# Kernel tuning notes

Hardware: AMD Instinct MI355X
Metric: run time of the kernel (lower is better)

## Reference

```python
import jax, jax.numpy as jnp
import numpy as np

GAMMA = 0.01
INFER_STEP = 3


def softor(x, axis, gamma=GAMMA):
    # smoothed logic-OR: gamma*logsumexp(x/gamma), normalized if it exceeds 1 (alphailp/NSFR semantics)
    lse = gamma * jax.nn.logsumexp(x / gamma, axis=axis)
    m = jnp.max(lse)
    return jnp.where(m > 1.0, lse / m, lse)


def clause_eval(R, I, gamma=GAMMA):
    # R: [C,B,G] per-clause valuations, I: [C,G,S,L] index tensor (values in [0,G))
    # gathered[c,b,g,s,l] = R[c, b, I[c,g,s,l]]
    gathered = jax.vmap(lambda Rc, Ic: jnp.take(Rc, Ic, axis=1))(R, I)  # [C,B,G,S,L]
    body = jnp.prod(gathered, axis=-1)  # product over body atoms L -> [C,B,G,S]
    return softor(body, axis=-1, gamma=gamma)  # soft-OR over substitutions S -> [C,B,G]


def setup_inputs() -> dict:
    key = jax.random.key(0)
    k1, k2 = jax.random.split(key)
    C, B, G, S, L = 4, 128, 2048, 32, 3
    x = jax.random.uniform(k1, (B, G), dtype=jnp.float32)  # atom valuations in [0,1]
    I = jax.random.randint(k2, (C, G, S, L), 0, G, dtype=jnp.int32)
    return {"x": x, "I": I}


def reference(x, I):
    C = I.shape[0]
    B, G = x.shape
    R = jnp.broadcast_to(x[None], (C, B, G))  # expand to per-clause valuation
    for _ in range(INFER_STEP):
        # amalgamate previous valuation with one inference step via soft-OR along stacked dim
        R = softor(jnp.stack([R, clause_eval(R, I)], axis=1), axis=1)
    return R
```

## Files before the change

kernel.cpp:

```cpp
#include <hip/hip_runtime.h>
#include <hip/hip_fp16.h>
#include <cstdint>
#include <cstddef>

#define C_ 4
#define B_ 128
#define G_ 2048
#define S_ 32
#define L_ 3
#define NSTEP_ 3
#define GAMMA_ 0.01f
#define INVG_LOG2E_ 144.26950408889634f
#define GAMMA_LN2_ 0.0069314718055994530942f

#define SLOT_U_ 256
#define BANK_U_ 32
__device__ __forceinline__ float slot_max(const uint32_t* slots, int slot) {
  float m = 0.0f;
#pragma unroll
  for (int k = 0; k < 8; ++k)
    m = fmaxf(m, __uint_as_float(slots[slot * SLOT_U_ + k * BANK_U_]));
  return m;
}

__global__ __launch_bounds__(256) void k_initT(const float* __restrict__ x,
                                               float* __restrict__ xT,
                                               __half* __restrict__ x16) {
  __shared__ float tile[32][33];
  const int g0 = blockIdx.x * 32, b0 = blockIdx.y * 32;
  const int tx = threadIdx.x;
  for (int i = threadIdx.y; i < 32; i += 8)
    tile[i][tx] = x[(size_t)(b0 + i) * G_ + g0 + tx];
  __syncthreads();
  for (int j = threadIdx.y; j < 32; j += 8) {
    const float v = tile[tx][j];
    xT[(size_t)(g0 + j) * B_ + b0 + tx] = v;
    x16[(size_t)(g0 + j) * B_ + b0 + tx] = __float2half_rn(v);
  }
}

__global__ __launch_bounds__(128) void k_gather(
    const __half* __restrict__ A16, size_t cstride,
    const int* __restrict__ Idx, float* __restrict__ Lout,
    uint32_t* slots, int prev_slot, int out_slot) {
  __shared__ int sidx[2 * S_ * L_];
  const int tid = threadIdx.x;
  const int lane = tid & 63;
  const int w = tid >> 6;
  const int bid = blockIdx.x;
  const int cgp = ((bid & 7) << 9) | (bid >> 3);
  const int cg = 2 * cgp + w;
  const int c = cg >> 11;

  for (int i = tid; i < 2 * S_ * L_; i += 128)
    sidx[i] = Idx[(size_t)(2 * cgp) * (S_ * L_) + i];
  const float mprev = slot_max(slots, prev_slot);
  const float scale = (mprev > 1.0f) ? (1.0f / mprev) : 1.0f;
  const float s3 = scale * scale * scale;
  const float K = s3 * INVG_LOG2E_;
  __syncthreads();

  const int* widx = sidx + w * (S_ * L_);
  const __half* Ac = A16 + (size_t)c * cstride;

  float M0 = -1.0f, M1 = -1.0f;
  float acc0 = 0.0f, acc1 = 0.0f;
#pragma unroll
  for (int s0 = 0; s0 < S_; s0 += 8) {
    __half2 v[24];
#pragma unroll
    for (int j = 0; j < 24; ++j) {
      const int row = __builtin_amdgcn_readfirstlane(widx[s0 * 3 + j]);
      v[j] =
          *reinterpret_cast<const __half2*>(Ac + (size_t)row * B_ + 2 * lane);
    }
    float b0[8], b1[8];
#pragma unroll
    for (int k = 0; k < 8; ++k) {
      const float2 f0 = __half22float2(v[3 * k + 0]);
      const float2 f1 = __half22float2(v[3 * k + 1]);
      const float2 f2 = __half22float2(v[3 * k + 2]);
      b0[k] = f0.x * f1.x * f2.x;
      b1[k] = f0.y * f1.y * f2.y;
    }
    float cm0 = b0[0], cm1 = b1[0];
#pragma unroll
    for (int k = 1; k < 8; ++k) {
      cm0 = fmaxf(cm0, b0[k]);
      cm1 = fmaxf(cm1, b1[k]);
    }
    const float Mn0 = fmaxf(M0, cm0);
    const float Mn1 = fmaxf(M1, cm1);
    acc0 *= exp2f((M0 - Mn0) * K);
    acc1 *= exp2f((M1 - Mn1) * K);
#pragma unroll
    for (int k = 0; k < 8; ++k) {
      acc0 += exp2f((b0[k] - Mn0) * K);
      acc1 += exp2f((b1[k] - Mn1) * K);
    }
    M0 = Mn0;
    M1 = Mn1;
  }
  const float lse0 = M0 * s3 + GAMMA_LN2_ * log2f(acc0);
  const float lse1 = M1 * s3 + GAMMA_LN2_ * log2f(acc1);
  *reinterpret_cast<float2*>(Lout + (size_t)cg * B_ + 2 * lane) =
      make_float2(lse0, lse1);

  float t = fmaxf(lse0, lse1);
#pragma unroll
  for (int off = 32; off >= 1; off >>= 1) t = fmaxf(t, __shfl_xor(t, off));
  if (lane == 0)
    atomicMax(slots + out_slot * SLOT_U_ + (bid & 7) * BANK_U_,
              __float_as_uint(t));
}

__global__ __launch_bounds__(256) void k_elem(
    const float* __restrict__ Rin, size_t rstride, float* __restrict__ A,
    __half* __restrict__ A16, const float* __restrict__ Lin, uint32_t* slots,
    int prev_slot, int m1_slot, int out_slot) {
  __shared__ float wmax[4];
  const float mprev = slot_max(slots, prev_slot);
  const float sprev = (mprev > 1.0f) ? (1.0f / mprev) : 1.0f;
  const float m1 = slot_max(slots, m1_slot);
  const float s1 = (m1 > 1.0f) ? (1.0f / m1) : 1.0f;

  const int e = (blockIdx.x * 256 + threadIdx.x) * 4;
  const int c = e >> 18;
  const int rem = e & (G_ * B_ - 1);
  const float4 Rv =
      *reinterpret_cast<const float4*>(Rin + (size_t)c * rstride + rem);
  const float4 Lv = *reinterpret_cast<const float4*>(Lin + e);

  float r[4] = {Rv.x, Rv.y, Rv.z, Rv.w};
  float l[4] = {Lv.x, Lv.y, Lv.z, Lv.w};
  float o[4];
  float tmax = 0.0f;
#pragma unroll
  for (int k = 0; k < 4; ++k) {
    const float R = r[k] * sprev;
    const float ce = l[k] * s1;
    const float M = fmaxf(R, ce);
    const float mn = fminf(R, ce);
    const float lse2 =
        M + GAMMA_LN2_ * log2f(1.0f + exp2f((mn - M) * INVG_LOG2E_));
    o[k] = lse2;
    tmax = fmaxf(tmax, lse2);
  }
  *reinterpret_cast<float4*>(A + e) = make_float4(o[0], o[1], o[2], o[3]);
  if (A16) {
    union {
      __half2 h[2];
      uint2 u;
    } pk;
    pk.h[0] = __floats2half2_rn(o[0], o[1]);
    pk.h[1] = __floats2half2_rn(o[2], o[3]);
    *reinterpret_cast<uint2*>(A16 + e) = pk.u;
  }

  float t = tmax;
#pragma unroll
  for (int off = 32; off >= 1; off >>= 1) t = fmaxf(t, __shfl_xor(t, off));
  if ((threadIdx.x & 63) == 0) wmax[threadIdx.x >> 6] = t;
  __syncthreads();
  if (threadIdx.x == 0) {
    const float bm = fmaxf(fmaxf(wmax[0], wmax[1]), fmaxf(wmax[2], wmax[3]));
    atomicMax(slots + out_slot * SLOT_U_ + (blockIdx.x & 7) * BANK_U_,
              __float_as_uint(bm));
  }
}

__global__ __launch_bounds__(256) void k_out(const float* __restrict__ A,
                                             float* __restrict__ out,
                                             const uint32_t* __restrict__ slots,
                                             int mslot) {
  __shared__ float tile[32][33];
  const float mfin = slot_max(slots, mslot);
  const float sc = (mfin > 1.0f) ? (1.0f / mfin) : 1.0f;
  const int g0 = blockIdx.x * 32, b0 = blockIdx.y * 32, c = blockIdx.z;
  const int tx = threadIdx.x;
  for (int j = threadIdx.y; j < 32; j += 8)
    tile[j][tx] = A[((size_t)c * G_ + g0 + j) * B_ + b0 + tx];
  __syncthreads();
  for (int i = threadIdx.y; i < 32; i += 8)
    out[((size_t)c * B_ + b0 + i) * G_ + g0 + tx] = tile[tx][i] * sc;
}

extern "C" void kernel_launch(void* const* d_in, const int* in_sizes, int n_in,
                              void* d_out, int out_size, void* d_ws,
                              size_t ws_size, hipStream_t stream) {
  const float* x = (const float*)d_in[0];
  const int* Idx = (const int*)d_in[1];
  float* out = (float*)d_out;

  const size_t CS = (size_t)G_ * B_;
  char* ws = (char*)d_ws;
  uint32_t* slots = (uint32_t*)ws;
  float* A = (float*)(ws + 16384);
  float* Lb = A + CS * C_;
  float* xT = Lb + CS * C_;
  __half* A16 = (__half*)(xT + CS);
  __half* x16 = A16 + CS * C_;

  hipMemsetAsync(slots, 0, 8192, stream);

  k_initT<<<dim3(G_ / 32, B_ / 32), dim3(32, 8), 0, stream>>>(x, xT, x16);

  for (int step = 0; step < NSTEP_; ++step) {
    const int prev = 2 * step;
    const int m1s = 2 * step + 1;
    const int m2s = 2 * step + 2;
    const __half* Gsrc = (step == 0) ? x16 : A16;
    const size_t gs = (step == 0) ? 0 : CS;
    const float* Rsrc = (step == 0) ? xT : A;
    const size_t rs = (step == 0) ? 0 : CS;
    __half* A16out = (step < NSTEP_ - 1) ? A16 : nullptr;
    k_gather<<<(C_ * G_) / 2, 128, 0, stream>>>(Gsrc, gs, Idx, Lb, slots, prev,
                                                m1s);
    k_elem<<<(C_ * G_ * B_) / (256 * 4), 256, 0, stream>>>(
        Rsrc, rs, A, A16out, Lb, slots, prev, m1s, m2s);
  }

  k_out<<<dim3(G_ / 32, B_ / 32, C_), dim3(32, 8), 0, stream>>>(A, out, slots,
                                                                2 * NSTEP_);
}
```

Before: 154.9 us.

## Fold slot reset into transpose kernel and load gather indices via registers

The separate memset of the max-reduction slots is removed; the first block of the transpose kernel now zeroes them, which saves one stream operation. The gather kernel moves from 2 to 4 waves per block. Each wave now loads its 96 clause indices as int4 values into lanes and broadcasts them with readlane, replacing the shared-memory staging and __syncthreads. The trade-off is more scalar readlane instructions and a different block-to-clause mapping, which may change cache locality for the row gathers.

```diff
diff --git a/kernel.cpp b/kernel.cpp
--- a/kernel.cpp
+++ b/kernel.cpp
@@ -25,7 +25,12 @@
 
 __global__ __launch_bounds__(256) void k_initT(const float* __restrict__ x,
                                                float* __restrict__ xT,
-                                               __half* __restrict__ x16) {
+                                               __half* __restrict__ x16,
+                                               uint32_t* __restrict__ slots) {
+  if (blockIdx.x == 0 && blockIdx.y == 0) {
+    const int t = threadIdx.y * 32 + threadIdx.x;
+    for (int i = t; i < 2048; i += 256) slots[i] = 0u;
+  }
   __shared__ float tile[32][33];
   const int g0 = blockIdx.x * 32, b0 = blockIdx.y * 32;
   const int tx = threadIdx.x;
@@ -39,28 +44,26 @@
   }
 }
 
-__global__ __launch_bounds__(128) void k_gather(
+__global__ __launch_bounds__(256) void k_gather(
     const __half* __restrict__ A16, size_t cstride,
     const int* __restrict__ Idx, float* __restrict__ Lout,
     uint32_t* slots, int prev_slot, int out_slot) {
-  __shared__ int sidx[2 * S_ * L_];
   const int tid = threadIdx.x;
   const int lane = tid & 63;
   const int w = tid >> 6;
   const int bid = blockIdx.x;
-  const int cgp = ((bid & 7) << 9) | (bid >> 3);
-  const int cg = 2 * cgp + w;
+  const int cg = ((bid & 7) << 10) | (((bid >> 3) << 2) | w);
   const int c = cg >> 11;
 
-  for (int i = tid; i < 2 * S_ * L_; i += 128)
-    sidx[i] = Idx[(size_t)(2 * cgp) * (S_ * L_) + i];
+  int4 idx4 = make_int4(0, 0, 0, 0);
+  const int4* Ip = reinterpret_cast<const int4*>(Idx + (size_t)cg * (S_ * L_));
+  if (lane < 24) idx4 = Ip[lane];
+
   const float mprev = slot_max(slots, prev_slot);
   const float scale = (mprev > 1.0f) ? (1.0f / mprev) : 1.0f;
   const float s3 = scale * scale * scale;
   const float K = s3 * INVG_LOG2E_;
-  __syncthreads();
-
-  const int* widx = sidx + w * (S_ * L_);
+
   const __half* Ac = A16 + (size_t)c * cstride;
 
   float M0 = -1.0f, M1 = -1.0f;
@@ -70,7 +73,18 @@
     __half2 v[24];
 #pragma unroll
     for (int j = 0; j < 24; ++j) {
-      const int row = __builtin_amdgcn_readfirstlane(widx[s0 * 3 + j]);
+      const int flat = s0 * 3 + j;
+      const int src = flat >> 2;
+      const int comp = flat & 3;
+      int row;
+      if (comp == 0)
+        row = __builtin_amdgcn_readlane(idx4.x, src);
+      else if (comp == 1)
+        row = __builtin_amdgcn_readlane(idx4.y, src);
+      else if (comp == 2)
+        row = __builtin_amdgcn_readlane(idx4.z, src);
+      else
+        row = __builtin_amdgcn_readlane(idx4.w, src);
       v[j] =
           *reinterpret_cast<const __half2*>(Ac + (size_t)row * B_ + 2 * lane);
     }
@@ -201,9 +215,8 @@
   __half* A16 = (__half*)(xT + CS);
   __half* x16 = A16 + CS * C_;
 
-  hipMemsetAsync(slots, 0, 8192, stream);
-
-  k_initT<<<dim3(G_ / 32, B_ / 32), dim3(32, 8), 0, stream>>>(x, xT, x16);
+  k_initT<<<dim3(G_ / 32, B_ / 32), dim3(32, 8), 0, stream>>>(x, xT, x16,
+                                                              slots);
 
   for (int step = 0; step < NSTEP_; ++step) {
     const int prev = 2 * step;
@@ -214,7 +227,7 @@
     const float* Rsrc = (step == 0) ? xT : A;
     const size_t rs = (step == 0) ? 0 : CS;
     __half* A16out = (step < NSTEP_ - 1) ? A16 : nullptr;
-    k_gather<<<(C_ * G_) / 2, 128, 0, stream>>>(Gsrc, gs, Idx, Lb, slots, prev,
+    k_gather<<<(C_ * G_) / 4, 256, 0, stream>>>(Gsrc, gs, Idx, Lb, slots, prev,
                                                 m1s);
     k_elem<<<(C_ * G_ * B_) / (256 * 4), 256, 0, stream>>>(
         Rsrc, rs, A, A16out, Lb, slots, prev, m1s, m2s);
```

Result: no change. 154.3 us (-0.4%).
